# Optimization experiments

Measured on AMD Instinct MI355X. Metric: run time of the kernel, lower is better.

The kernel has to match this reference:

```python
import jax, jax.numpy as jnp
import numpy as np

CR = 32  # channels // reduction

def setup_inputs() -> dict:
    key = jax.random.key(0)
    k1, k2 = jax.random.split(key)
    x = jax.random.normal(k1, (1, 64, 8, 32, 32), dtype=jnp.float32)
    W = jax.random.normal(k2, (CR, 64), dtype=jnp.float32) * (1.0 / np.sqrt(64.0))
    bias = jnp.zeros((CR,), dtype=jnp.float32)
    return {"x": x, "W": W, "bias": bias}

def reference(x, W, bias):
    b, c, d, h, w = x.shape
    cr = W.shape[0]
    n = d * h * w
    # 1x1x1 Conv3d == per-voxel linear projection over channels
    x_red = jnp.einsum('oc,bcdhw->bodhw', W, x) + bias[None, :, None, None, None]
    q = x_red.reshape(b, cr, n)          # [b, cr, N]
    k = q                                 # shared projection (q == k)
    v = x.reshape(b, c, n)               # [b, c, N]
    # attn[b, i, j] = <q[:, i], k[:, j]>, softmax over j (dim=2)
    attn = jnp.einsum('bci,bcj->bij', q, k) / jnp.sqrt(jnp.float32(cr))
    attn = jax.nn.softmax(attn, axis=2)
    # out[b, c, m] = sum_n v[b, c, n] * attn[b, n, m]  (torch.bmm(v, attn))
    out = jnp.einsum('bcn,bnm->bcm', v, attn)
    out = out.reshape(b, c, d, h, w)
    return out + x
```

## Files before the change

### kernel.cpp

```cpp
#include <hip/hip_runtime.h>

#define N_TOK 8192

typedef _Float16 f16x8 __attribute__((ext_vector_type(8)));
typedef _Float16 f16x4 __attribute__((ext_vector_type(4)));
typedef float    f32x4 __attribute__((ext_vector_type(4)));

__device__ __forceinline__ f32x4 mfma16(f16x8 a, f16x8 b, f32x4 c) {
  return __builtin_amdgcn_mfma_f32_16x16x32_f16(a, b, c, 0, 0, 0);
}

#define QSCALE 0.50500977f

__global__ __launch_bounds__(256) void prep_kernel(
    const float* __restrict__ x, const float* __restrict__ W,
    const float* __restrict__ bias, _Float16* __restrict__ qe,
    _Float16* __restrict__ vh) {
  int blk = blockIdx.x, t = threadIdx.x;
  if (blk < 1024) {
    __shared__ float Wl[32 * 65];
    for (int i = t; i < 2048; i += 256) Wl[(i >> 6) * 65 + (i & 63)] = W[i];
    __syncthreads();
    int g = blk * 256 + t;
    int o = g & 31, n = g >> 5;
    float acc0 = bias[o], acc1 = 0.f;
#pragma unroll
    for (int c = 0; c < 32; ++c) {
      acc0 = fmaf(Wl[o * 65 + c], x[c * N_TOK + n], acc0);
      acc1 = fmaf(Wl[o * 65 + 32 + c], x[(32 + c) * N_TOK + n], acc1);
    }
    qe[n * 32 + o] = (_Float16)((acc0 + acc1) * QSCALE);
  } else {
    int i4 = (blk - 1024) * 256 + t;
    f32x4 v = ((const f32x4*)x)[i4];
    f16x4 h;
#pragma unroll
    for (int j = 0; j < 4; ++j) h[j] = (_Float16)v[j];
    *(f16x4*)(vh + i4 * 4) = h;
  }
}

__global__ __launch_bounds__(512) void pass1_kernel(
    const _Float16* __restrict__ qe, float* __restrict__ Bn) {
  __shared__ float Lp[8][32];
  int t = threadIdx.x;
  int w = t >> 6, lane = t & 63, quad = lane >> 4, l15 = lane & 15;
  int n0 = blockIdx.x * 32;
  f16x8 af0 = *(const f16x8*)(qe + (n0 + l15) * 32 + quad * 8);
  f16x8 af1 = *(const f16x8*)(qe + (n0 + 16 + l15) * 32 + quad * 8);
  f32x4 sums0 = {0.f, 0.f, 0.f, 0.f}, sums1 = {0.f, 0.f, 0.f, 0.f};
  for (int mt = 0; mt < 64; ++mt) {
    int m0 = w * 1024 + mt * 16;
    f16x8 bf = *(const f16x8*)(qe + (m0 + l15) * 32 + quad * 8);
    f32x4 zero = {0.f, 0.f, 0.f, 0.f};
    f32x4 s0 = mfma16(af0, bf, zero);
    f32x4 s1 = mfma16(af1, bf, zero);
#pragma unroll
    for (int r = 0; r < 4; ++r) {
      sums0[r] += __builtin_amdgcn_exp2f(s0[r]);
      sums1[r] += __builtin_amdgcn_exp2f(s1[r]);
    }
  }
#pragma unroll
  for (int r = 0; r < 4; ++r) {
#pragma unroll
    for (int mask = 1; mask < 16; mask <<= 1) {
      sums0[r] += __shfl_xor(sums0[r], mask, 64);
      sums1[r] += __shfl_xor(sums1[r], mask, 64);
    }
  }
  if (l15 == 0) {
    *(f32x4*)&Lp[w][quad * 4] = sums0;
    *(f32x4*)&Lp[w][16 + quad * 4] = sums1;
  }
  __syncthreads();
  if (t < 32) {
    float L = 0.f;
#pragma unroll
    for (int ww = 0; ww < 8; ++ww) L += Lp[ww][t];
    Bn[n0 + t] = __builtin_amdgcn_logf(L);
  }
}

__global__ __launch_bounds__(1024) void pass2_kernel(
    const _Float16* __restrict__ qe, const _Float16* __restrict__ vh,
    const float* __restrict__ Bn, const float* __restrict__ x,
    float* __restrict__ out) {
  __shared__ _Float16 Pt[16 * 1280];
  __shared__ float Ot[8 * 64 * 33];
  int t = threadIdx.x;
  int w = t >> 6, lane = t & 63, quad = lane >> 4, l15 = lane & 15;
  int m0 = blockIdx.x * 32;
  _Float16* myP = Pt + w * 1280;

  f16x8 bm0 = *(const f16x8*)(qe + (m0 + l15) * 32 + quad * 8);
  f16x8 bm1 = *(const f16x8*)(qe + (m0 + 16 + l15) * 32 + quad * 8);

  f32x4 acc[4][2];
#pragma unroll
  for (int ct = 0; ct < 4; ++ct)
#pragma unroll
    for (int mt = 0; mt < 2; ++mt) acc[ct][mt] = f32x4{0.f, 0.f, 0.f, 0.f};

  for (int ch = 0; ch < 16; ++ch) {
    int nb = w * 512 + ch * 32;
    f16x8 an[2];
    an[0] = *(const f16x8*)(qe + (nb + l15) * 32 + quad * 8);
    an[1] = *(const f16x8*)(qe + (nb + 16 + l15) * 32 + quad * 8);
    f32x4 Bq[2];
    Bq[0] = *(const f32x4*)(Bn + nb + quad * 4);
    Bq[1] = *(const f32x4*)(Bn + nb + 16 + quad * 4);
    __asm__ volatile("s_waitcnt lgkmcnt(0)" ::: "memory");
#pragma unroll
    for (int nt = 0; nt < 2; ++nt) {
      f16x8 a = an[nt];
#pragma unroll
      for (int mt = 0; mt < 2; ++mt) {
        f32x4 zero = {0.f, 0.f, 0.f, 0.f};
        f32x4 s = mfma16(a, (mt == 0) ? bm0 : bm1, zero);
        f16x4 p;
#pragma unroll
        for (int r = 0; r < 4; ++r)
          p[r] = (_Float16)__builtin_amdgcn_exp2f(s[r] - Bq[nt][r]);
        *(f16x4*)(myP + (mt * 16 + l15) * 40 + nt * 16 + quad * 4) = p;
      }
    }
    __asm__ volatile("s_waitcnt lgkmcnt(0)" ::: "memory");
    f16x8 bp0 = *(const f16x8*)(myP + l15 * 40 + quad * 8);
    f16x8 bp1 = *(const f16x8*)(myP + (16 + l15) * 40 + quad * 8);
#pragma unroll
    for (int ct = 0; ct < 4; ++ct) {
      f16x8 av = *(const f16x8*)(vh + (ct * 16 + l15) * N_TOK + nb + quad * 8);
      acc[ct][0] = mfma16(av, bp0, acc[ct][0]);
      acc[ct][1] = mfma16(av, bp1, acc[ct][1]);
    }
  }

  if (w < 8) {
#pragma unroll
    for (int ct = 0; ct < 4; ++ct)
#pragma unroll
      for (int mt = 0; mt < 2; ++mt)
#pragma unroll
        for (int r = 0; r < 4; ++r)
          Ot[(w * 64 + ct * 16 + quad * 4 + r) * 33 + mt * 16 + l15] =
              acc[ct][mt][r];
  }
  __syncthreads();
  if (w >= 8) {
#pragma unroll
    for (int ct = 0; ct < 4; ++ct)
#pragma unroll
      for (int mt = 0; mt < 2; ++mt)
#pragma unroll
        for (int r = 0; r < 4; ++r)
          Ot[((w - 8) * 64 + ct * 16 + quad * 4 + r) * 33 + mt * 16 + l15] +=
              acc[ct][mt][r];
  }
  __syncthreads();
  for (int idx = t; idx < 2048; idx += 1024) {
    int cc = idx >> 5, m = idx & 31;
    float v = 0.f;
#pragma unroll
    for (int s = 0; s < 8; ++s) v += Ot[(s * 64 + cc) * 33 + m];
    out[cc * N_TOK + m0 + m] = v + x[cc * N_TOK + m0 + m];
  }
}

extern "C" void kernel_launch(void* const* d_in, const int* in_sizes, int n_in,
                              void* d_out, int out_size, void* d_ws,
                              size_t ws_size, hipStream_t stream) {
  const float* x = (const float*)d_in[0];
  const float* W = (const float*)d_in[1];
  const float* bias = (const float*)d_in[2];
  float* out = (float*)d_out;

  char* ws = (char*)d_ws;
  _Float16* qe = (_Float16*)ws;
  _Float16* vh = (_Float16*)(ws + 524288);
  float* Bn = (float*)(ws + 524288 + 1048576);

  prep_kernel<<<1536, 256, 0, stream>>>(x, W, bias, qe, vh);
  pass1_kernel<<<256, 512, 0, stream>>>(qe, Bn);
  pass2_kernel<<<256, 1024, 0, stream>>>(qe, vh, Bn, x, out);
}
```

Before: 114.2 us.

## Keep softmax probabilities in registers via 16x16x16 MFMA and widen pass1 blocks

New measurement: 142.9 us. +25.2%, slower.

```diff
diff --git a/kernel.cpp b/kernel.cpp
--- a/kernel.cpp
+++ b/kernel.cpp
@@ -6,8 +6,11 @@
 typedef _Float16 f16x4 __attribute__((ext_vector_type(4)));
 typedef float    f32x4 __attribute__((ext_vector_type(4)));
 
-__device__ __forceinline__ f32x4 mfma16(f16x8 a, f16x8 b, f32x4 c) {
+__device__ __forceinline__ f32x4 mfma_k32(f16x8 a, f16x8 b, f32x4 c) {
   return __builtin_amdgcn_mfma_f32_16x16x32_f16(a, b, c, 0, 0, 0);
+}
+__device__ __forceinline__ f32x4 mfma_k16(f16x4 a, f16x4 b, f32x4 c) {
+  return __builtin_amdgcn_mfma_f32_16x16x16f16(a, b, c, 0, 0, 0);
 }
 
 #define QSCALE 0.50500977f
@@ -40,21 +43,21 @@
   }
 }
 
-__global__ __launch_bounds__(512) void pass1_kernel(
+__global__ __launch_bounds__(1024) void pass1_kernel(
     const _Float16* __restrict__ qe, float* __restrict__ Bn) {
-  __shared__ float Lp[8][32];
+  __shared__ float Lp[16][32];
   int t = threadIdx.x;
   int w = t >> 6, lane = t & 63, quad = lane >> 4, l15 = lane & 15;
   int n0 = blockIdx.x * 32;
   f16x8 af0 = *(const f16x8*)(qe + (n0 + l15) * 32 + quad * 8);
   f16x8 af1 = *(const f16x8*)(qe + (n0 + 16 + l15) * 32 + quad * 8);
   f32x4 sums0 = {0.f, 0.f, 0.f, 0.f}, sums1 = {0.f, 0.f, 0.f, 0.f};
-  for (int mt = 0; mt < 64; ++mt) {
-    int m0 = w * 1024 + mt * 16;
+  for (int mt = 0; mt < 32; ++mt) {
+    int m0 = w * 512 + mt * 16;
     f16x8 bf = *(const f16x8*)(qe + (m0 + l15) * 32 + quad * 8);
     f32x4 zero = {0.f, 0.f, 0.f, 0.f};
-    f32x4 s0 = mfma16(af0, bf, zero);
-    f32x4 s1 = mfma16(af1, bf, zero);
+    f32x4 s0 = mfma_k32(af0, bf, zero);
+    f32x4 s1 = mfma_k32(af1, bf, zero);
 #pragma unroll
     for (int r = 0; r < 4; ++r) {
       sums0[r] += __builtin_amdgcn_exp2f(s0[r]);
@@ -77,7 +80,7 @@
   if (t < 32) {
     float L = 0.f;
 #pragma unroll
-    for (int ww = 0; ww < 8; ++ww) L += Lp[ww][t];
+    for (int ww = 0; ww < 16; ++ww) L += Lp[ww][t];
     Bn[n0 + t] = __builtin_amdgcn_logf(L);
   }
 }
@@ -86,12 +89,10 @@
     const _Float16* __restrict__ qe, const _Float16* __restrict__ vh,
     const float* __restrict__ Bn, const float* __restrict__ x,
     float* __restrict__ out) {
-  __shared__ _Float16 Pt[16 * 1280];
   __shared__ float Ot[8 * 64 * 33];
   int t = threadIdx.x;
   int w = t >> 6, lane = t & 63, quad = lane >> 4, l15 = lane & 15;
   int m0 = blockIdx.x * 32;
-  _Float16* myP = Pt + w * 1280;
 
   f16x8 bm0 = *(const f16x8*)(qe + (m0 + l15) * 32 + quad * 8);
   f16x8 bm1 = *(const f16x8*)(qe + (m0 + 16 + l15) * 32 + quad * 8);
@@ -102,37 +103,28 @@
 #pragma unroll
     for (int mt = 0; mt < 2; ++mt) acc[ct][mt] = f32x4{0.f, 0.f, 0.f, 0.f};
 
-  for (int ch = 0; ch < 16; ++ch) {
-    int nb = w * 512 + ch * 32;
-    f16x8 an[2];
-    an[0] = *(const f16x8*)(qe + (nb + l15) * 32 + quad * 8);
-    an[1] = *(const f16x8*)(qe + (nb + 16 + l15) * 32 + quad * 8);
-    f32x4 Bq[2];
-    Bq[0] = *(const f32x4*)(Bn + nb + quad * 4);
-    Bq[1] = *(const f32x4*)(Bn + nb + 16 + quad * 4);
-    __asm__ volatile("s_waitcnt lgkmcnt(0)" ::: "memory");
+  for (int ch = 0; ch < 32; ++ch) {
+    int nb = w * 512 + ch * 16;
+    f16x8 a = *(const f16x8*)(qe + (nb + l15) * 32 + quad * 8);
+    f32x4 Bq = *(const f32x4*)(Bn + nb + quad * 4);
+    f16x4 av[4];
 #pragma unroll
-    for (int nt = 0; nt < 2; ++nt) {
-      f16x8 a = an[nt];
+    for (int ct = 0; ct < 4; ++ct)
+      av[ct] = *(const f16x4*)(vh + (ct * 16 + l15) * N_TOK + nb + quad * 4);
+
+    f32x4 zero = {0.f, 0.f, 0.f, 0.f};
+    f32x4 s0 = mfma_k32(a, bm0, zero);
+    f32x4 s1 = mfma_k32(a, bm1, zero);
+    f16x4 p0, p1;
 #pragma unroll
-      for (int mt = 0; mt < 2; ++mt) {
-        f32x4 zero = {0.f, 0.f, 0.f, 0.f};
-        f32x4 s = mfma16(a, (mt == 0) ? bm0 : bm1, zero);
-        f16x4 p;
-#pragma unroll
-        for (int r = 0; r < 4; ++r)
-          p[r] = (_Float16)__builtin_amdgcn_exp2f(s[r] - Bq[nt][r]);
-        *(f16x4*)(myP + (mt * 16 + l15) * 40 + nt * 16 + quad * 4) = p;
-      }
+    for (int r = 0; r < 4; ++r) {
+      p0[r] = (_Float16)__builtin_amdgcn_exp2f(s0[r] - Bq[r]);
+      p1[r] = (_Float16)__builtin_amdgcn_exp2f(s1[r] - Bq[r]);
     }
-    __asm__ volatile("s_waitcnt lgkmcnt(0)" ::: "memory");
-    f16x8 bp0 = *(const f16x8*)(myP + l15 * 40 + quad * 8);
-    f16x8 bp1 = *(const f16x8*)(myP + (16 + l15) * 40 + quad * 8);
 #pragma unroll
     for (int ct = 0; ct < 4; ++ct) {
-      f16x8 av = *(const f16x8*)(vh + (ct * 16 + l15) * N_TOK + nb + quad * 8);
-      acc[ct][0] = mfma16(av, bp0, acc[ct][0]);
-      acc[ct][1] = mfma16(av, bp1, acc[ct][1]);
+      acc[ct][0] = mfma_k16(av[ct], p0, acc[ct][0]);
+      acc[ct][1] = mfma_k16(av[ct], p1, acc[ct][1]);
     }
   }
 
@@ -181,6 +173,6 @@
   float* Bn = (float*)(ws + 524288 + 1048576);
 
   prep_kernel<<<1536, 256, 0, stream>>>(x, W, bias, qe, vh);
-  pass1_kernel<<<256, 512, 0, stream>>>(qe, Bn);
+  pass1_kernel<<<256, 1024, 0, stream>>>(qe, Bn);
   pass2_kernel<<<256, 1024, 0, stream>>>(qe, vh, Bn, x, out);
 }
```
